# Performance work log

Measured on AMD Instinct MI355X. Metric: run time of the kernel, lower is better.

The kernel has to match this reference:

```python
import jax, jax.numpy as jnp
import numpy as np

B = 2048          # num_graphs
N_PER = 68        # landmarks per graph
DEG = 8           # avg degree -> 544 edges per graph
E_PER = N_PER * DEG
F_IN, F_HID, N_CLUST = 2, 128, 8


def setup_inputs() -> dict:
    key = jax.random.key(0)
    ks = jax.random.split(key, 16)
    N = B * N_PER
    x = jax.random.normal(ks[0], (N, F_IN), dtype=jnp.float32)
    # intra-graph random edges: local ids in [0,68) + per-graph offset
    local = jax.random.randint(ks[1], (2, B, E_PER), 0, N_PER)
    offs = (jnp.arange(B, dtype=jnp.int64) * N_PER)[None, :, None]
    edge_index = (local.astype(jnp.int64) + offs).reshape(2, -1)
    adj = jax.random.uniform(ks[2], (B, N_PER, N_PER), dtype=jnp.float32)
    s = jax.random.normal(ks[3], (B, N_PER, N_CLUST), dtype=jnp.float32)
    def lin(k, fi, fo):
        return jax.random.normal(k, (fi, fo), dtype=jnp.float32) / np.sqrt(fi)
    return {
        'x': x, 'edge_index': edge_index, 'adj': adj, 's': s,
        'W_root1': lin(ks[4], F_IN, F_HID), 'W_rel1': lin(ks[5], F_IN, F_HID),
        'b1': jnp.zeros((F_HID,), jnp.float32),
        'W_root2': lin(ks[6], F_HID, F_HID), 'W_rel2': lin(ks[7], F_HID, F_HID),
        'b2': jnp.zeros((F_HID,), jnp.float32),
        'W_root3': lin(ks[8], F_HID, F_HID), 'W_rel3': lin(ks[9], F_HID, F_HID),
        'b3': jnp.zeros((F_HID,), jnp.float32),
        'fc_w': lin(ks[10], F_HID, 1), 'fc_b': jnp.zeros((1,), jnp.float32),
    }


def _graph_conv(x, src, dst, W_root, W_rel, b, num_nodes):
    # PyG GraphConv (aggr='add'): out_i = W_rel @ sum_{j->i} x_j + W_root @ x_i + b
    agg = jax.ops.segment_sum(x[src], dst, num_segments=num_nodes)
    return agg @ W_rel + x @ W_root + b


def reference(x, edge_index, adj, s,
              W_root1, W_rel1, b1, W_root2, W_rel2, b2,
              W_root3, W_rel3, b3, fc_w, fc_b):
    N = x.shape[0]
    src, dst = edge_index[0], edge_index[1]
    h = jax.nn.relu(_graph_conv(x, src, dst, W_root1, W_rel1, b1, N))
    h = jax.nn.relu(_graph_conv(h, src, dst, W_root2, W_rel2, b2, N))
    h = jax.nn.relu(_graph_conv(h, src, dst, W_root3, W_rel3, b3, N))
    bsz = adj.shape[0]
    xr = h.reshape(bsz, N_PER, F_HID)            # [B,68,128]
    s_sm = jax.nn.softmax(s, axis=-1)            # dense_diff_pool softmax
    xp = jnp.einsum('bnc,bnf->bcf', s_sm, xr)    # pooled features [B,8,128]
    # (pooled adj / link / entropy losses are computed then discarded in the
    #  original forward; they do not affect the returned value -> omitted)
    # MaxPool2d((1,8)) over [B,8,128] -> [B,8,16]
    pooled = xp.reshape(bsz, N_CLUST, F_HID // 8, 8).max(axis=-1)
    flat = pooled.reshape(bsz, -1)               # [B,128]
    return flat @ fc_w + fc_b                    # [B,1]
```

## Files before the change

kernel.cpp:

```cpp
#include <hip/hip_runtime.h>
#include <hip/hip_bf16.h>

#define NPER 68
#define EPER 544
#define FH   128
#define NC   8
#define AJW  104
#define HTW  88

#define SMEM_TOTAL 75360
#define OFF_HT   34816
#define OFF_ADJ  57344
#define OFF_ST   71488
#define OFF_XL   74816

typedef short short8 __attribute__((ext_vector_type(8)));
typedef float f32x4 __attribute__((ext_vector_type(4)));
typedef unsigned short ushort4v __attribute__((ext_vector_type(4)));

__device__ __forceinline__ unsigned short f2bf(float f) {
    unsigned int u = __float_as_uint(f);
    return (unsigned short)((u + 0x7FFFu + ((u >> 16) & 1u)) >> 16);
}
__device__ __forceinline__ unsigned short f2bf_c(float f) {
    __hip_bfloat16 b = __float2bfloat16(f);
    return __builtin_bit_cast(unsigned short, b);
}
__device__ __forceinline__ float bf2f(unsigned short h) {
    return __uint_as_float(((unsigned int)h) << 16);
}
__device__ __forceinline__ unsigned int swzB(unsigned int row, unsigned int bc) {
    return row * 512u + (bc ^ (((row ^ (row >> 3)) & 7u) << 4));
}

__global__ void pack_w(const float* __restrict__ Wrel2, const float* __restrict__ Wroot2,
                       const float* __restrict__ Wrel3, const float* __restrict__ Wroot3,
                       unsigned short* __restrict__ ws) {
    int o = blockIdx.x * 256 + threadIdx.x;
    int j = o & 7, l = (o >> 3) & 63, n = (o >> 9) & 7, t = (o >> 12) & 7, L = o >> 15;
    int k = t * 32 + ((l >> 4) << 3) + j;
    int f = n * 16 + (l & 15);
    const float* Wl = L ? Wrel3 : Wrel2;
    const float* Wr = L ? Wroot3 : Wroot2;
    float v = (k < FH) ? Wl[k * FH + f] : Wr[(k - FH) * FH + f];
    ws[o] = f2bf(v);
}

__launch_bounds__(256, 2)
__global__ void gnn_kernel(const float* __restrict__ x,
                           const int*   __restrict__ ei,
                           const float* __restrict__ s,
                           const float* __restrict__ Wroot1, const float* __restrict__ Wrel1,
                           const float* __restrict__ b1,
                           const float* __restrict__ b2, const float* __restrict__ b3,
                           const unsigned short* __restrict__ wpack,
                           const float* __restrict__ fcw, const float* __restrict__ fcb,
                           float* __restrict__ out, int nE)
{
    __shared__ __align__(16) char smem[SMEM_TOTAL];
    unsigned short* bcat = (unsigned short*)smem;
    unsigned short* hT   = (unsigned short*)(smem + OFF_HT);
    unsigned short* adjb = (unsigned short*)(smem + OFF_ADJ);
    unsigned short* sT   = (unsigned short*)(smem + OFF_ST);
    float*          xl   = (float*)(smem + OFF_XL);

    const int g = blockIdx.x, tid = threadIdx.x, lane = tid & 63, wid = tid >> 6;
    const int gnode = g * NPER, gedge = g * EPER;
    const int* srcp = ei;
    const int* dstp = ei + nE;
    unsigned int* adj32 = (unsigned int*)adjb;
    unsigned int* sT32  = (unsigned int*)sT;
    unsigned int* h32   = (unsigned int*)bcat;
    unsigned int* ht32  = (unsigned int*)hT;

    for (int i = tid; i < NPER * (AJW / 2); i += 256) adj32[i] = 0u;
    for (int i = tid; i < 8 * (AJW / 2); i += 256) sT32[i] = 0u;
    for (int i = tid; i < NPER * 32; i += 256)
        h32[(i >> 5) * 128 + (i & 31)] = 0u;
    for (int i = tid; i < 128 * 10; i += 256)
        ht32[(i / 10) * (HTW / 2) + 34 + (i % 10)] = 0u;
    for (int i = tid; i < NPER * 2; i += 256) xl[i] = x[gnode * 2 + i];
    __syncthreads();

    for (int e = tid; e < EPER; e += 256) {
        int s_ = srcp[gedge + e] - gnode;
        int d_ = dstp[gedge + e] - gnode;
        int idx = d_ * AJW + s_;
        atomicAdd(&adj32[idx >> 1], (idx & 1) ? 0x10000u : 1u);
    }
    __syncthreads();
    for (int i = tid; i < NPER * (AJW / 2); i += 256) {
        unsigned int u = adj32[i];
        if (u) {
            adj32[i] = (unsigned int)f2bf((float)(u & 0xffffu))
                     | ((unsigned int)f2bf((float)(u >> 16)) << 16);
        }
    }
    __syncthreads();

    if (tid < 136) {
        int i = tid >> 1, ft = tid & 1;
        float a = 0.f;
        for (int j = 0; j < NPER; ++j) a += bf2f(adjb[i * AJW + j]) * xl[j * 2 + ft];
        *(unsigned short*)((char*)bcat + swzB(i, ft * 2))     = f2bf(a);
        *(unsigned short*)((char*)bcat + swzB(i, 4 + ft * 2)) = f2bf(xl[i * 2 + ft]);
    } else if (tid < 204) {
        int i = tid - 136;
        float v[NC]; float m = -1e30f;
        #pragma unroll
        for (int c = 0; c < NC; ++c) { v[c] = s[(gnode + i) * NC + c]; m = fmaxf(m, v[c]); }
        float sum = 0.f;
        #pragma unroll
        for (int c = 0; c < NC; ++c) { v[c] = __expf(v[c] - m); sum += v[c]; }
        float inv = 1.f / sum;
        #pragma unroll
        for (int c = 0; c < NC; ++c) sT[c * AJW + i] = f2bf(v[c] * inv);
    }
    __syncthreads();

    const int arow = lane & 15, aq = lane >> 4, akB = aq * 16, akE = aq * 8;

    auto epilogue_h = [&](f32x4 (&acc)[5][2], const float* __restrict__ bv) {
        #pragma unroll
        for (int c2 = 0; c2 < 2; ++c2) {
            int f = (wid * 2 + c2) * 16 + arow;
            float bias = bv[f];
            #pragma unroll
            for (int m = 0; m < 5; ++m) {
                int rbase = m * 16 + aq * 4;
                if (rbase < NPER) {
                    ushort4v w;
                    #pragma unroll
                    for (int i2 = 0; i2 < 4; ++i2) {
                        float v = acc[m][c2][i2] + bias;
                        v = v > 0.f ? v : 0.f;
                        unsigned short us = f2bf_c(v);
                        w[i2] = us;
                        *(unsigned short*)((char*)bcat + swzB(rbase + i2, (FH + f) * 2)) = us;
                    }
                    *(ushort4v*)(hT + f * HTW + rbase) = w;
                }
            }
        }
    };

    {
        f32x4 acc[5][2];
        #pragma unroll
        for (int m = 0; m < 5; ++m) { acc[m][0] = (f32x4)0.f; acc[m][1] = (f32x4)0.f; }
        short8 bf[2];
        #pragma unroll
        for (int c2 = 0; c2 < 2; ++c2) {
            int f = (wid * 2 + c2) * 16 + arow;
            #pragma unroll
            for (int j = 0; j < 8; ++j) {
                float wv = 0.f;
                if (aq == 0) {
                    if (j < 2) wv = Wrel1[j * FH + f];
                    else if (j < 4) wv = Wroot1[(j - 2) * FH + f];
                }
                bf[c2][j] = (short)f2bf(wv);
            }
        }
        #pragma unroll
        for (int m = 0; m < 5; ++m) {
            short8 a = *(const short8*)((char*)bcat + swzB(m * 16 + arow, akB));
            acc[m][0] = __builtin_amdgcn_mfma_f32_16x16x32_bf16(a, bf[0], acc[m][0], 0, 0, 0);
            acc[m][1] = __builtin_amdgcn_mfma_f32_16x16x32_bf16(a, bf[1], acc[m][1], 0, 0, 0);
        }
        epilogue_h(acc, b1);
    }
    __syncthreads();

    #pragma unroll 1
    for (int L = 0; L < 2; ++L) {
        f32x4 acc[5][2];
        #pragma unroll
        for (int m = 0; m < 5; ++m) { acc[m][0] = (f32x4)0.f; acc[m][1] = (f32x4)0.f; }
        #pragma unroll
        for (int kt = 0; kt < 3; ++kt) {
            int cb = kt * 32 + akE; if (cb >= HTW) cb = 0;
            short8 bg[2];
            #pragma unroll
            for (int c2 = 0; c2 < 2; ++c2) {
                int f = (wid * 2 + c2) * 16 + arow;
                bg[c2] = *(const short8*)(hT + f * HTW + cb);
            }
            #pragma unroll
            for (int m = 0; m < 5; ++m) {
                short8 a = *(const short8*)(adjb + (m * 16 + arow) * AJW + kt * 32 + akE);
                acc[m][0] = __builtin_amdgcn_mfma_f32_16x16x32_bf16(a, bg[0], acc[m][0], 0, 0, 0);
                acc[m][1] = __builtin_amdgcn_mfma_f32_16x16x32_bf16(a, bg[1], acc[m][1], 0, 0, 0);
            }
        }
        #pragma unroll
        for (int c2 = 0; c2 < 2; ++c2) {
            int f = (wid * 2 + c2) * 16 + arow;
            #pragma unroll
            for (int m = 0; m < 5; ++m) {
                int rbase = m * 16 + aq * 4;
                if (rbase < NPER) {
                    #pragma unroll
                    for (int i2 = 0; i2 < 4; ++i2)
                        *(unsigned short*)((char*)bcat + swzB(rbase + i2, f * 2)) = f2bf_c(acc[m][c2][i2]);
                }
            }
        }
        __syncthreads();

        f32x4 acc2[5][2];
        #pragma unroll
        for (int m = 0; m < 5; ++m) { acc2[m][0] = (f32x4)0.f; acc2[m][1] = (f32x4)0.f; }
        const unsigned short* wsL = wpack + (L << 15);
        for (int t = 0; t < 8; ++t) {
            short8 bf0 = *(const short8*)(wsL + (((t * 8 + wid * 2 + 0) * 64 + lane) << 3));
            short8 bf1 = *(const short8*)(wsL + (((t * 8 + wid * 2 + 1) * 64 + lane) << 3));
            #pragma unroll
            for (int m = 0; m < 5; ++m) {
                short8 a = *(const short8*)((char*)bcat + swzB(m * 16 + arow, t * 64 + akB));
                acc2[m][0] = __builtin_amdgcn_mfma_f32_16x16x32_bf16(a, bf0, acc2[m][0], 0, 0, 0);
                acc2[m][1] = __builtin_amdgcn_mfma_f32_16x16x32_bf16(a, bf1, acc2[m][1], 0, 0, 0);
            }
        }
        __syncthreads();
        epilogue_h(acc2, L ? b3 : b2);
        __syncthreads();
    }

    float* xpf = (float*)(smem + OFF_ADJ);
    {
        f32x4 accp[2]; accp[0] = (f32x4)0.f; accp[1] = (f32x4)0.f;
        #pragma unroll
        for (int kt = 0; kt < 3; ++kt) {
            int cb = kt * 32 + akE; if (cb >= HTW) cb = 0;
            short8 bg[2];
            #pragma unroll
            for (int c2 = 0; c2 < 2; ++c2) {
                int f = (wid * 2 + c2) * 16 + arow;
                bg[c2] = *(const short8*)(hT + f * HTW + cb);
            }
            short8 a = *(const short8*)(sT + arow * AJW + kt * 32 + akE);
            accp[0] = __builtin_amdgcn_mfma_f32_16x16x32_bf16(a, bg[0], accp[0], 0, 0, 0);
            accp[1] = __builtin_amdgcn_mfma_f32_16x16x32_bf16(a, bg[1], accp[1], 0, 0, 0);
        }
        #pragma unroll
        for (int c2 = 0; c2 < 2; ++c2) {
            int f = (wid * 2 + c2) * 16 + arow;
            if (aq < 2) {
                #pragma unroll
                for (int i2 = 0; i2 < 4; ++i2) xpf[(aq * 4 + i2) * FH + f] = accp[c2][i2];
            }
        }
    }
    __syncthreads();

    float* red = xpf + NC * FH;
    float partial = 0.f;
    if (tid < 128) {
        int c = tid >> 4, q = tid & 15;
        float m = xpf[c * FH + q * 8];
        #pragma unroll
        for (int j = 1; j < 8; ++j) m = fmaxf(m, xpf[c * FH + q * 8 + j]);
        partial = m * fcw[tid];
    }
    if (tid < 128) red[tid] = partial;
    __syncthreads();
    if (tid < 64) {
        float v = red[tid] + red[tid + 64];
        #pragma unroll
        for (int off = 32; off > 0; off >>= 1) v += __shfl_down(v, off, 64);
        if (tid == 0) out[g] = v + fcb[0];
    }
}

extern "C" void kernel_launch(void* const* d_in, const int* in_sizes, int n_in,
                              void* d_out, int out_size, void* d_ws, size_t ws_size,
                              hipStream_t stream) {
    const float* x      = (const float*)d_in[0];
    const int*   ei     = (const int*)d_in[1];
    const float* s      = (const float*)d_in[3];
    const float* Wroot1 = (const float*)d_in[4];
    const float* Wrel1  = (const float*)d_in[5];
    const float* b1     = (const float*)d_in[6];
    const float* Wroot2 = (const float*)d_in[7];
    const float* Wrel2  = (const float*)d_in[8];
    const float* b2     = (const float*)d_in[9];
    const float* Wroot3 = (const float*)d_in[10];
    const float* Wrel3  = (const float*)d_in[11];
    const float* b3     = (const float*)d_in[12];
    const float* fcw    = (const float*)d_in[13];
    const float* fcb    = (const float*)d_in[14];
    float* out = (float*)d_out;
    unsigned short* wpack = (unsigned short*)d_ws;

    const int nE = in_sizes[1] / 2;
    const int B  = in_sizes[3] / (NPER * NC);

    pack_w<<<256, 256, 0, stream>>>(Wrel2, Wroot2, Wrel3, Wroot3, wpack);
    gnn_kernel<<<B, 256, 0, stream>>>(x, ei, s,
                                      Wroot1, Wrel1, b1,
                                      b2, b3, wpack,
                                      fcw, fcb, out, nE);
}
```

Measured before the change: 180.4 us.

## Double block size to 512 threads, one 16-column feature tile per wave

Launches 8 waves per graph instead of 4, with each wave computing a single 16-wide output feature tile rather than two. This halves per-wave accumulator registers and MFMA chains, raising the number of resident waves to hide LDS and memory latency. In exchange, the A-operand fragments are loaded from LDS by twice as many waves, and barriers synchronize larger blocks.

```diff
diff --git a/kernel.cpp b/kernel.cpp
--- a/kernel.cpp
+++ b/kernel.cpp
@@ -7,6 +7,7 @@
 #define NC   8
 #define AJW  104
 #define HTW  88
+#define NT   512
 
 #define SMEM_TOTAL 75360
 #define OFF_HT   34816
@@ -46,7 +47,7 @@
     ws[o] = f2bf(v);
 }
 
-__launch_bounds__(256, 2)
+__launch_bounds__(NT, 2)
 __global__ void gnn_kernel(const float* __restrict__ x,
                            const int*   __restrict__ ei,
                            const float* __restrict__ s,
@@ -73,23 +74,23 @@
     unsigned int* h32   = (unsigned int*)bcat;
     unsigned int* ht32  = (unsigned int*)hT;
 
-    for (int i = tid; i < NPER * (AJW / 2); i += 256) adj32[i] = 0u;
-    for (int i = tid; i < 8 * (AJW / 2); i += 256) sT32[i] = 0u;
-    for (int i = tid; i < NPER * 32; i += 256)
+    for (int i = tid; i < NPER * (AJW / 2); i += NT) adj32[i] = 0u;
+    for (int i = tid; i < 8 * (AJW / 2); i += NT) sT32[i] = 0u;
+    for (int i = tid; i < NPER * 32; i += NT)
         h32[(i >> 5) * 128 + (i & 31)] = 0u;
-    for (int i = tid; i < 128 * 10; i += 256)
+    for (int i = tid; i < 128 * 10; i += NT)
         ht32[(i / 10) * (HTW / 2) + 34 + (i % 10)] = 0u;
-    for (int i = tid; i < NPER * 2; i += 256) xl[i] = x[gnode * 2 + i];
-    __syncthreads();
-
-    for (int e = tid; e < EPER; e += 256) {
+    for (int i = tid; i < NPER * 2; i += NT) xl[i] = x[gnode * 2 + i];
+    __syncthreads();
+
+    for (int e = tid; e < EPER; e += NT) {
         int s_ = srcp[gedge + e] - gnode;
         int d_ = dstp[gedge + e] - gnode;
         int idx = d_ * AJW + s_;
         atomicAdd(&adj32[idx >> 1], (idx & 1) ? 0x10000u : 1u);
     }
     __syncthreads();
-    for (int i = tid; i < NPER * (AJW / 2); i += 256) {
+    for (int i = tid; i < NPER * (AJW / 2); i += NT) {
         unsigned int u = adj32[i];
         if (u) {
             adj32[i] = (unsigned int)f2bf((float)(u & 0xffffu))
@@ -119,54 +120,46 @@
     __syncthreads();
 
     const int arow = lane & 15, aq = lane >> 4, akB = aq * 16, akE = aq * 8;
-
-    auto epilogue_h = [&](f32x4 (&acc)[5][2], const float* __restrict__ bv) {
-        #pragma unroll
-        for (int c2 = 0; c2 < 2; ++c2) {
-            int f = (wid * 2 + c2) * 16 + arow;
-            float bias = bv[f];
-            #pragma unroll
-            for (int m = 0; m < 5; ++m) {
-                int rbase = m * 16 + aq * 4;
-                if (rbase < NPER) {
-                    ushort4v w;
-                    #pragma unroll
-                    for (int i2 = 0; i2 < 4; ++i2) {
-                        float v = acc[m][c2][i2] + bias;
-                        v = v > 0.f ? v : 0.f;
-                        unsigned short us = f2bf_c(v);
-                        w[i2] = us;
-                        *(unsigned short*)((char*)bcat + swzB(rbase + i2, (FH + f) * 2)) = us;
-                    }
-                    *(ushort4v*)(hT + f * HTW + rbase) = w;
+    const int fcol = wid * 16 + arow;
+
+    auto epilogue_h = [&](f32x4 (&acc)[5], const float* __restrict__ bv) {
+        float bias = bv[fcol];
+        #pragma unroll
+        for (int m = 0; m < 5; ++m) {
+            int rbase = m * 16 + aq * 4;
+            if (rbase < NPER) {
+                ushort4v w;
+                #pragma unroll
+                for (int i2 = 0; i2 < 4; ++i2) {
+                    float v = acc[m][i2] + bias;
+                    v = v > 0.f ? v : 0.f;
+                    unsigned short us = f2bf_c(v);
+                    w[i2] = us;
+                    *(unsigned short*)((char*)bcat + swzB(rbase + i2, (FH + fcol) * 2)) = us;
                 }
+                *(ushort4v*)(hT + fcol * HTW + rbase) = w;
             }
         }
     };
 
     {
-        f32x4 acc[5][2];
-        #pragma unroll
-        for (int m = 0; m < 5; ++m) { acc[m][0] = (f32x4)0.f; acc[m][1] = (f32x4)0.f; }
-        short8 bf[2];
-        #pragma unroll
-        for (int c2 = 0; c2 < 2; ++c2) {
-            int f = (wid * 2 + c2) * 16 + arow;
-            #pragma unroll
-            for (int j = 0; j < 8; ++j) {
-                float wv = 0.f;
-                if (aq == 0) {
-                    if (j < 2) wv = Wrel1[j * FH + f];
-                    else if (j < 4) wv = Wroot1[(j - 2) * FH + f];
-                }
-                bf[c2][j] = (short)f2bf(wv);
-            }
+        f32x4 acc[5];
+        #pragma unroll
+        for (int m = 0; m < 5; ++m) acc[m] = (f32x4)0.f;
+        short8 bf;
+        #pragma unroll
+        for (int j = 0; j < 8; ++j) {
+            float wv = 0.f;
+            if (aq == 0) {
+                if (j < 2) wv = Wrel1[j * FH + fcol];
+                else if (j < 4) wv = Wroot1[(j - 2) * FH + fcol];
+            }
+            bf[j] = (short)f2bf(wv);
         }
         #pragma unroll
         for (int m = 0; m < 5; ++m) {
             short8 a = *(const short8*)((char*)bcat + swzB(m * 16 + arow, akB));
-            acc[m][0] = __builtin_amdgcn_mfma_f32_16x16x32_bf16(a, bf[0], acc[m][0], 0, 0, 0);
-            acc[m][1] = __builtin_amdgcn_mfma_f32_16x16x32_bf16(a, bf[1], acc[m][1], 0, 0, 0);
+            acc[m] = __builtin_amdgcn_mfma_f32_16x16x32_bf16(a, bf, acc[m], 0, 0, 0);
         }
         epilogue_h(acc, b1);
     }
@@ -174,52 +167,40 @@
 
     #pragma unroll 1
     for (int L = 0; L < 2; ++L) {
-        f32x4 acc[5][2];
-        #pragma unroll
-        for (int m = 0; m < 5; ++m) { acc[m][0] = (f32x4)0.f; acc[m][1] = (f32x4)0.f; }
+        f32x4 acc[5];
+        #pragma unroll
+        for (int m = 0; m < 5; ++m) acc[m] = (f32x4)0.f;
         #pragma unroll
         for (int kt = 0; kt < 3; ++kt) {
             int cb = kt * 32 + akE; if (cb >= HTW) cb = 0;
-            short8 bg[2];
-            #pragma unroll
-            for (int c2 = 0; c2 < 2; ++c2) {
-                int f = (wid * 2 + c2) * 16 + arow;
-                bg[c2] = *(const short8*)(hT + f * HTW + cb);
-            }
+            short8 bg = *(const short8*)(hT + fcol * HTW + cb);
             #pragma unroll
             for (int m = 0; m < 5; ++m) {
                 short8 a = *(const short8*)(adjb + (m * 16 + arow) * AJW + kt * 32 + akE);
-                acc[m][0] = __builtin_amdgcn_mfma_f32_16x16x32_bf16(a, bg[0], acc[m][0], 0, 0, 0);
-                acc[m][1] = __builtin_amdgcn_mfma_f32_16x16x32_bf16(a, bg[1], acc[m][1], 0, 0, 0);
-            }
-        }
-        #pragma unroll
-        for (int c2 = 0; c2 < 2; ++c2) {
-            int f = (wid * 2 + c2) * 16 + arow;
-            #pragma unroll
-            for (int m = 0; m < 5; ++m) {
-                int rbase = m * 16 + aq * 4;
-                if (rbase < NPER) {
-                    #pragma unroll
-                    for (int i2 = 0; i2 < 4; ++i2)
-                        *(unsigned short*)((char*)bcat + swzB(rbase + i2, f * 2)) = f2bf_c(acc[m][c2][i2]);
-                }
+                acc[m] = __builtin_amdgcn_mfma_f32_16x16x32_bf16(a, bg, acc[m], 0, 0, 0);
+            }
+        }
+        #pragma unroll
+        for (int m = 0; m < 5; ++m) {
+            int rbase = m * 16 + aq * 4;
+            if (rbase < NPER) {
+                #pragma unroll
+                for (int i2 = 0; i2 < 4; ++i2)
+                    *(unsigned short*)((char*)bcat + swzB(rbase + i2, fcol * 2)) = f2bf_c(acc[m][i2]);
             }
         }
         __syncthreads();
 
-        f32x4 acc2[5][2];
-        #pragma unroll
-        for (int m = 0; m < 5; ++m) { acc2[m][0] = (f32x4)0.f; acc2[m][1] = (f32x4)0.f; }
+        f32x4 acc2[5];
+        #pragma unroll
+        for (int m = 0; m < 5; ++m) acc2[m] = (f32x4)0.f;
         const unsigned short* wsL = wpack + (L << 15);
         for (int t = 0; t < 8; ++t) {
-            short8 bf0 = *(const short8*)(wsL + (((t * 8 + wid * 2 + 0) * 64 + lane) << 3));
-            short8 bf1 = *(const short8*)(wsL + (((t * 8 + wid * 2 + 1) * 64 + lane) << 3));
+            short8 bf0 = *(const short8*)(wsL + (((t * 8 + wid) * 64 + lane) << 3));
             #pragma unroll
             for (int m = 0; m < 5; ++m) {
                 short8 a = *(const short8*)((char*)bcat + swzB(m * 16 + arow, t * 64 + akB));
-                acc2[m][0] = __builtin_amdgcn_mfma_f32_16x16x32_bf16(a, bf0, acc2[m][0], 0, 0, 0);
-                acc2[m][1] = __builtin_amdgcn_mfma_f32_16x16x32_bf16(a, bf1, acc2[m][1], 0, 0, 0);
+                acc2[m] = __builtin_amdgcn_mfma_f32_16x16x32_bf16(a, bf0, acc2[m], 0, 0, 0);
             }
         }
         __syncthreads();
@@ -229,27 +210,17 @@
 
     float* xpf = (float*)(smem + OFF_ADJ);
     {
-        f32x4 accp[2]; accp[0] = (f32x4)0.f; accp[1] = (f32x4)0.f;
+        f32x4 accp = (f32x4)0.f;
         #pragma unroll
         for (int kt = 0; kt < 3; ++kt) {
             int cb = kt * 32 + akE; if (cb >= HTW) cb = 0;
-            short8 bg[2];
+            short8 bg = *(const short8*)(hT + fcol * HTW + cb);
+            short8 a = *(const short8*)(sT + arow * AJW + kt * 32 + akE);
+            accp = __builtin_amdgcn_mfma_f32_16x16x32_bf16(a, bg, accp, 0, 0, 0);
+        }
+        if (aq < 2) {
             #pragma unroll
-            for (int c2 = 0; c2 < 2; ++c2) {
-                int f = (wid * 2 + c2) * 16 + arow;
-                bg[c2] = *(const short8*)(hT + f * HTW + cb);
-            }
-            short8 a = *(const short8*)(sT + arow * AJW + kt * 32 + akE);
-            accp[0] = __builtin_amdgcn_mfma_f32_16x16x32_bf16(a, bg[0], accp[0], 0, 0, 0);
-            accp[1] = __builtin_amdgcn_mfma_f32_16x16x32_bf16(a, bg[1], accp[1], 0, 0, 0);
-        }
-        #pragma unroll
-        for (int c2 = 0; c2 < 2; ++c2) {
-            int f = (wid * 2 + c2) * 16 + arow;
-            if (aq < 2) {
-                #pragma unroll
-                for (int i2 = 0; i2 < 4; ++i2) xpf[(aq * 4 + i2) * FH + f] = accp[c2][i2];
-            }
+            for (int i2 = 0; i2 < 4; ++i2) xpf[(aq * 4 + i2) * FH + fcol] = accp[i2];
         }
     }
     __syncthreads();
@@ -297,8 +268,8 @@
     const int B  = in_sizes[3] / (NPER * NC);
 
     pack_w<<<256, 256, 0, stream>>>(Wrel2, Wroot2, Wrel3, Wroot3, wpack);
-    gnn_kernel<<<B, 256, 0, stream>>>(x, ei, s,
-                                      Wroot1, Wrel1, b1,
-                                      b2, b3, wpack,
-                                      fcw, fcb, out, nE);
-}
+    gnn_kernel<<<B, NT, 0, stream>>>(x, ei, s,
+                                     Wroot1, Wrel1, b1,
+                                     b2, b3, wpack,
+                                     fcw, fcb, out, nE);
+}
```

Measured after the change: 203.6 us. 12.9% more time.
